# Optimization experiments

Measured on AMD Instinct MI355X. Metric: run time of the kernel, lower is better.

## Reference

```python
import jax, jax.numpy as jnp
import numpy as np

N_ENTITY = 64368
N_REL = 40
DIM = 128
N_BASES = 8
N_EDGES = 500000
BATCH = 64
SEED_LEN = 32


def _glorot(k, shape, gain=1.414):
    fan_in, fan_out = shape[0], shape[1]
    bound = gain * np.sqrt(6.0 / (fan_in + fan_out))
    return jax.random.uniform(k, shape, jnp.float32, -bound, bound)


def setup_inputs() -> dict:
    key = jax.random.key(0)
    ks = jax.random.split(key, 11)
    return dict(
        seed_ids=jax.random.randint(ks[0], (BATCH, SEED_LEN), 0, N_ENTITY),
        edge_src=jax.random.randint(ks[1], (N_EDGES,), 0, N_ENTITY),
        edge_dst=jax.random.randint(ks[2], (N_EDGES,), 0, N_ENTITY),
        edge_type=jax.random.randint(ks[3], (N_EDGES,), 0, N_REL),
        basis=jax.random.normal(ks[4], (N_BASES, N_ENTITY, DIM), jnp.float32) * 0.02,
        att=jax.random.normal(ks[5], (N_REL, N_BASES), jnp.float32) * 0.1,
        root=jax.random.normal(ks[6], (N_ENTITY, DIM), jnp.float32) * 0.02,
        rgcn_bias=jnp.zeros((DIM,), jnp.float32),
        attn_a=_glorot(ks[7], (DIM, DIM)),
        attn_b=_glorot(ks[8], (DIM, 1)),
        out_bias=jnp.zeros((N_ENTITY,), jnp.float32),
    )


def _rgcn_nodes(basis, att, root, rgcn_bias, edge_src, edge_dst, edge_type):
    # RGCNConv with x=None: message for edge e is row src[e] of w[type[e]],
    # where w = att @ basis (basis decomposition); 'mean' aggregation to dst;
    # update: aggr + root + bias.
    n_entity, dim = root.shape
    coeff = att[edge_type]  # [E, nb]
    agg = jnp.zeros((n_entity, dim), jnp.float32)
    for b in range(basis.shape[0]):  # small fixed loop over bases
        m = basis[b][edge_src] * coeff[:, b][:, None]  # [E, dim]
        agg = agg + jax.ops.segment_sum(m, edge_dst, num_segments=n_entity)
    deg = jax.ops.segment_sum(jnp.ones_like(edge_dst, jnp.float32), edge_dst,
                              num_segments=n_entity)
    agg = agg / jnp.maximum(deg, 1.0)[:, None]
    return agg + root + rgcn_bias[None, :]


def reference(seed_ids, edge_src, edge_dst, edge_type, basis, att, root,
              rgcn_bias, attn_a, attn_b, out_bias):
    nodes = _rgcn_nodes(basis, att, root, rgcn_bias, edge_src, edge_dst, edge_type)
    # self-attention pooling over each seed set (all entries valid / non-empty)
    H = nodes[seed_ids]  # [B, S, D]
    e = jnp.einsum('bsd,d->bs', jnp.tanh(jnp.einsum('bsd,de->bse', H, attn_a)),
                   attn_b[:, 0])  # [B, S]
    attn = jax.nn.softmax(e, axis=-1)
    u = jnp.einsum('bs,bsd->bd', attn, H)  # [B, D]
    # scores = F.linear(u, nodes_features, output.bias)
    scores = u @ nodes.T + out_bias[None, :]  # [B, n_entity]
    return scores
```

## Files before the change

kernel.cpp:

```cpp
#include <hip/hip_runtime.h>
#include <hip/hip_fp16.h>

#define N_ENTITY 64368
#define N_REL 40
#define DIM 128
#define N_BASES 8
#define N_EDGES 500000
#define BATCH 64
#define SEED_LEN 32
#define NROWS (BATCH * SEED_LEN)
#define SCAN_NB ((N_ENTITY + 255) / 256)
#define NPAD (SCAN_NB * 256)

#define CAP_S 40
#define CAP_D 40

struct alignas(8) half4 { __half2 lo, hi; };

__global__ __launch_bounds__(256) void k_scatter(
    const int* __restrict__ esrc, const int* __restrict__ edst,
    const int* __restrict__ etype, const float* __restrict__ basis,
    const float* __restrict__ att, int* __restrict__ cnts,
    int* __restrict__ cntd, int* __restrict__ slots,
    __half* __restrict__ msg, float* __restrict__ agg)
{
    int e = blockIdx.x * 256 + threadIdx.x;
    if (e >= N_EDGES) return;
    int s = esrc[e], d = edst[e], t = etype[e];

    int kd = atomicAdd(&cntd[d], 1);
    unsigned pack;
    if (kd < CAP_D) pack = ((unsigned)(d * CAP_D + kd) << 6) | (unsigned)t;
    else            pack = 0x80000000u | ((unsigned)d << 6) | (unsigned)t;

    int ks = atomicAdd(&cnts[s], 1);
    if (ks < CAP_S) {
        slots[(size_t)s * CAP_S + ks] = (int)pack;
    } else {
        const size_t bstride = (size_t)N_ENTITY * DIM;
        for (int dd = 0; dd < DIM; ++dd) {
            float m = 0.f;
            #pragma unroll
            for (int b = 0; b < N_BASES; ++b)
                m += att[t * N_BASES + b] * basis[b * bstride + (size_t)s * DIM + dd];
            if (kd < CAP_D)
                msg[(size_t)(d * CAP_D + kd) * DIM + dd] = __float2half(m);
            else
                unsafeAtomicAdd(&agg[(size_t)d * DIM + dd], m);
        }
    }
}

__global__ __launch_bounds__(256) void k_phaseA(
    const int* __restrict__ cnts, const int* __restrict__ slots,
    const float* __restrict__ basis, const float* __restrict__ att,
    __half* __restrict__ msg, float* __restrict__ agg)
{
    __shared__ float att_s[N_REL * N_BASES];
    int tid = threadIdx.x;
    for (int i = tid; i < N_REL * N_BASES; i += 256) att_s[i] = att[i];
    __syncthreads();

    int sid = (blockIdx.x * 256 + tid) >> 5;
    int l32 = tid & 31;
    if (sid >= N_ENTITY) return;
    int cnt = cnts[sid];
    if (cnt == 0) return;
    if (cnt > CAP_S) cnt = CAP_S;
    const int* sl = slots + (size_t)sid * CAP_S;

    const size_t bstride = (size_t)N_ENTITY * DIM;
    const float* bp = basis + (size_t)sid * DIM + l32 * 4;
    float4 r0 = *(const float4*)(bp + 0 * bstride);
    float4 r1 = *(const float4*)(bp + 1 * bstride);
    float4 r2 = *(const float4*)(bp + 2 * bstride);
    float4 r3 = *(const float4*)(bp + 3 * bstride);
    float4 r4 = *(const float4*)(bp + 4 * bstride);
    float4 r5 = *(const float4*)(bp + 5 * bstride);
    float4 r6 = *(const float4*)(bp + 6 * bstride);
    float4 r7 = *(const float4*)(bp + 7 * bstride);

    int j = 0;
    for (; j + 1 < cnt; j += 2) {
        int pA = sl[j];
        int pB = sl[j + 1];
        const float* cAp = att_s + (pA & 63) * N_BASES;
        const float* cBp = att_s + (pB & 63) * N_BASES;
        float4 cA0 = *(const float4*)(cAp);
        float4 cA1 = *(const float4*)(cAp + 4);
        float4 cB0 = *(const float4*)(cBp);
        float4 cB1 = *(const float4*)(cBp + 4);

        float4 mA, mB;
        mA.x = cA0.x*r0.x + cA0.y*r1.x + cA0.z*r2.x + cA0.w*r3.x
             + cA1.x*r4.x + cA1.y*r5.x + cA1.z*r6.x + cA1.w*r7.x;
        mA.y = cA0.x*r0.y + cA0.y*r1.y + cA0.z*r2.y + cA0.w*r3.y
             + cA1.x*r4.y + cA1.y*r5.y + cA1.z*r6.y + cA1.w*r7.y;
        mA.z = cA0.x*r0.z + cA0.y*r1.z + cA0.z*r2.z + cA0.w*r3.z
             + cA1.x*r4.z + cA1.y*r5.z + cA1.z*r6.z + cA1.w*r7.z;
        mA.w = cA0.x*r0.w + cA0.y*r1.w + cA0.z*r2.w + cA0.w*r3.w
             + cA1.x*r4.w + cA1.y*r5.w + cA1.z*r6.w + cA1.w*r7.w;
        mB.x = cB0.x*r0.x + cB0.y*r1.x + cB0.z*r2.x + cB0.w*r3.x
             + cB1.x*r4.x + cB1.y*r5.x + cB1.z*r6.x + cB1.w*r7.x;
        mB.y = cB0.x*r0.y + cB0.y*r1.y + cB0.z*r2.y + cB0.w*r3.y
             + cB1.x*r4.y + cB1.y*r5.y + cB1.z*r6.y + cB1.w*r7.y;
        mB.z = cB0.x*r0.z + cB0.y*r1.z + cB0.z*r2.z + cB0.w*r3.z
             + cB1.x*r4.z + cB1.y*r5.z + cB1.z*r6.z + cB1.w*r7.z;
        mB.w = cB0.x*r0.w + cB0.y*r1.w + cB0.z*r2.w + cB0.w*r3.w
             + cB1.x*r4.w + cB1.y*r5.w + cB1.z*r6.w + cB1.w*r7.w;

        half4 hA, hB;
        hA.lo = __floats2half2_rn(mA.x, mA.y);
        hA.hi = __floats2half2_rn(mA.z, mA.w);
        hB.lo = __floats2half2_rn(mB.x, mB.y);
        hB.hi = __floats2half2_rn(mB.z, mB.w);
        if (pA >= 0) {
            *(half4*)(msg + ((size_t)((unsigned)pA >> 6) << 7) + (l32 << 2)) = hA;
        } else {
            int dd = (int)(((unsigned)pA >> 6) & 0x1FFFFu);
            float* ap = agg + (size_t)dd * DIM + l32 * 4;
            unsafeAtomicAdd(ap + 0, mA.x); unsafeAtomicAdd(ap + 1, mA.y);
            unsafeAtomicAdd(ap + 2, mA.z); unsafeAtomicAdd(ap + 3, mA.w);
        }
        if (pB >= 0) {
            *(half4*)(msg + ((size_t)((unsigned)pB >> 6) << 7) + (l32 << 2)) = hB;
        } else {
            int dd = (int)(((unsigned)pB >> 6) & 0x1FFFFu);
            float* ap = agg + (size_t)dd * DIM + l32 * 4;
            unsafeAtomicAdd(ap + 0, mB.x); unsafeAtomicAdd(ap + 1, mB.y);
            unsafeAtomicAdd(ap + 2, mB.z); unsafeAtomicAdd(ap + 3, mB.w);
        }
    }
    if (j < cnt) {
        int pA = sl[j];
        const float* cAp = att_s + (pA & 63) * N_BASES;
        float4 cA0 = *(const float4*)(cAp);
        float4 cA1 = *(const float4*)(cAp + 4);
        float4 mA;
        mA.x = cA0.x*r0.x + cA0.y*r1.x + cA0.z*r2.x + cA0.w*r3.x
             + cA1.x*r4.x + cA1.y*r5.x + cA1.z*r6.x + cA1.w*r7.x;
        mA.y = cA0.x*r0.y + cA0.y*r1.y + cA0.z*r2.y + cA0.w*r3.y
             + cA1.x*r4.y + cA1.y*r5.y + cA1.z*r6.y + cA1.w*r7.y;
        mA.z = cA0.x*r0.z + cA0.y*r1.z + cA0.z*r2.z + cA0.w*r3.z
             + cA1.x*r4.z + cA1.y*r5.z + cA1.z*r6.z + cA1.w*r7.z;
        mA.w = cA0.x*r0.w + cA0.y*r1.w + cA0.z*r2.w + cA0.w*r3.w
             + cA1.x*r4.w + cA1.y*r5.w + cA1.z*r6.w + cA1.w*r7.w;
        half4 hA;
        hA.lo = __floats2half2_rn(mA.x, mA.y);
        hA.hi = __floats2half2_rn(mA.z, mA.w);
        if (pA >= 0) {
            *(half4*)(msg + ((size_t)((unsigned)pA >> 6) << 7) + (l32 << 2)) = hA;
        } else {
            int dd = (int)(((unsigned)pA >> 6) & 0x1FFFFu);
            float* ap = agg + (size_t)dd * DIM + l32 * 4;
            unsafeAtomicAdd(ap + 0, mA.x); unsafeAtomicAdd(ap + 1, mA.y);
            unsafeAtomicAdd(ap + 2, mA.z); unsafeAtomicAdd(ap + 3, mA.w);
        }
    }
}

__global__ __launch_bounds__(256) void k_phaseB(
    const int* __restrict__ cntd, const __half* __restrict__ msg,
    const float* __restrict__ root, const float* __restrict__ bias,
    float* __restrict__ agg)
{
    int wid  = (int)((blockIdx.x * 256 + threadIdx.x) >> 6);
    int lane = threadIdx.x & 63;
    if (wid >= N_ENTITY) return;
    int c = cntd[wid];
    int n = (c < CAP_D) ? c : CAP_D;
    const __half2* mp = (const __half2*)msg + (size_t)wid * (CAP_D * 64) + lane;

    float ax = 0.f, ay = 0.f;
    int j = 0;
    for (; j + 3 < n; j += 4) {
        float2 f0 = __half22float2(mp[(j + 0) * 64]);
        float2 f1 = __half22float2(mp[(j + 1) * 64]);
        float2 f2 = __half22float2(mp[(j + 2) * 64]);
        float2 f3 = __half22float2(mp[(j + 3) * 64]);
        ax += (f0.x + f1.x) + (f2.x + f3.x);
        ay += (f0.y + f1.y) + (f2.y + f3.y);
    }
    for (; j < n; ++j) {
        float2 f = __half22float2(mp[j * 64]);
        ax += f.x; ay += f.y;
    }

    int o = wid * DIM + lane * 2;
    float2 prev = *(const float2*)(agg + o);
    ax += prev.x; ay += prev.y;

    float inv = 1.0f / fmaxf((float)c, 1.0f);
    float2 r  = *(const float2*)(root + o);
    float2 bb = *(const float2*)(bias + lane * 2);
    float2 outv;
    outv.x = ax * inv + r.x + bb.x;
    outv.y = ay * inv + r.y + bb.y;
    *(float2*)(agg + o) = outv;
}

__global__ __launch_bounds__(256) void k_attn(
    const int* __restrict__ seed_ids, const float* __restrict__ nodes,
    const float* __restrict__ A, const float* __restrict__ Bv,
    float* __restrict__ uT)
{
    __shared__ float Hs[SEED_LEN * DIM];
    __shared__ float ew[SEED_LEN];
    __shared__ float attw[SEED_LEN];

    int b = blockIdx.x, tid = threadIdx.x;

    for (int i = tid; i < SEED_LEN * DIM; i += 256) {
        int ss = i >> 7, d = i & 127;
        Hs[i] = nodes[(size_t)seed_ids[b * SEED_LEN + ss] * DIM + d];
    }
    __syncthreads();

    int jx = tid & 31;
    int iy = tid >> 5;
    float acc[4][4] = {{0,0,0,0},{0,0,0,0},{0,0,0,0},{0,0,0,0}};

    for (int d = 0; d < DIM; ++d) {
        const float4 a4 = *(const float4*)(A + d * DIM + jx * 4);
        float h0 = Hs[(iy * 4 + 0) * DIM + d];
        float h1 = Hs[(iy * 4 + 1) * DIM + d];
        float h2 = Hs[(iy * 4 + 2) * DIM + d];
        float h3 = Hs[(iy * 4 + 3) * DIM + d];
        acc[0][0] += h0 * a4.x; acc[0][1] += h0 * a4.y;
        acc[0][2] += h0 * a4.z; acc[0][3] += h0 * a4.w;
        acc[1][0] += h1 * a4.x; acc[1][1] += h1 * a4.y;
        acc[1][2] += h1 * a4.z; acc[1][3] += h1 * a4.w;
        acc[2][0] += h2 * a4.x; acc[2][1] += h2 * a4.y;
        acc[2][2] += h2 * a4.z; acc[2][3] += h2 * a4.w;
        acc[3][0] += h3 * a4.x; acc[3][1] += h3 * a4.y;
        acc[3][2] += h3 * a4.z; acc[3][3] += h3 * a4.w;
    }

    const float4 bv = *(const float4*)(Bv + jx * 4);
    #pragma unroll
    for (int i = 0; i < 4; ++i) {
        float pe = tanhf(acc[i][0]) * bv.x + tanhf(acc[i][1]) * bv.y
                 + tanhf(acc[i][2]) * bv.z + tanhf(acc[i][3]) * bv.w;
        pe += __shfl_xor(pe, 1, 64);
        pe += __shfl_xor(pe, 2, 64);
        pe += __shfl_xor(pe, 4, 64);
        pe += __shfl_xor(pe, 8, 64);
        pe += __shfl_xor(pe, 16, 64);
        if (jx == 0) ew[iy * 4 + i] = pe;
    }
    __syncthreads();

    if (tid == 0) {
        float mx = -1e30f;
        for (int k = 0; k < SEED_LEN; ++k) mx = fmaxf(mx, ew[k]);
        float ssum = 0.0f;
        for (int k = 0; k < SEED_LEN; ++k) {
            float v = expf(ew[k] - mx);
            attw[k] = v; ssum += v;
        }
        float inv = 1.0f / ssum;
        for (int k = 0; k < SEED_LEN; ++k) attw[k] *= inv;
    }
    __syncthreads();

    if (tid < DIM) {
        float a = 0.0f;
        for (int k = 0; k < SEED_LEN; ++k) a += attw[k] * Hs[k * DIM + tid];
        uT[tid * BATCH + b] = a;
    }
}

__global__ __launch_bounds__(256) void k_scores(
    const float* __restrict__ nodes, const float* __restrict__ uT,
    const float* __restrict__ out_bias, float* __restrict__ out)
{
    __shared__ float Nl[DIM * 65];

    int tid = threadIdx.x;
    int n0  = blockIdx.x * 64;

    for (int i = tid; i < 64 * DIM; i += 256) {
        int n = i >> 7, d = i & 127;
        int gn = n0 + n;
        Nl[d * 65 + n] = (gn < N_ENTITY) ? nodes[(size_t)gn * DIM + d] : 0.0f;
    }
    __syncthreads();

    int w    = __builtin_amdgcn_readfirstlane(tid >> 6);
    int lane = tid & 63;
    int b0   = w * 16;

    float acc[16];
    #pragma unroll
    for (int k = 0; k < 16; ++k) acc[k] = 0.0f;

    #pragma unroll 4
    for (int d = 0; d < DIM; ++d) {
        float nv = Nl[d * 65 + lane];
        const float* up = uT + d * BATCH + b0;
        #pragma unroll
        for (int k = 0; k < 16; ++k) acc[k] += up[k] * nv;
    }

    int gn = n0 + lane;
    if (gn < N_ENTITY) {
        float ob = out_bias[gn];
        #pragma unroll
        for (int k = 0; k < 16; ++k)
            out[(size_t)(b0 + k) * N_ENTITY + gn] = acc[k] + ob;
    }
}

__global__ __launch_bounds__(256) void k_histF(
    const int* __restrict__ edst, int* __restrict__ hist)
{
    int e = blockIdx.x * 256 + threadIdx.x;
    if (e < N_EDGES) atomicAdd(&hist[edst[e]], 1);
}

__global__ __launch_bounds__(256) void k_scan1F(
    const int* __restrict__ hist, int* __restrict__ ptr,
    int* __restrict__ partial)
{
    __shared__ int s[256];
    int tid = threadIdx.x;
    int gid = blockIdx.x * 256 + tid;
    int v = hist[gid];
    s[tid] = v;
    __syncthreads();
    for (int off = 1; off < 256; off <<= 1) {
        int t = (tid >= off) ? s[tid - off] : 0;
        __syncthreads();
        s[tid] += t;
        __syncthreads();
    }
    ptr[gid] = s[tid] - v;
    if (tid == 255) partial[blockIdx.x] = s[255];
}

__global__ __launch_bounds__(256) void k_scan23F(
    int* __restrict__ ptr, const int* __restrict__ partial,
    int* __restrict__ work)
{
    __shared__ int s[256];
    int tid = threadIdx.x;
    int c   = blockIdx.x;
    int sum = 0;
    for (int k = tid; k < c; k += 256) sum += partial[k];
    s[tid] = sum;
    __syncthreads();
    for (int off = 128; off > 0; off >>= 1) {
        if (tid < off) s[tid] += s[tid + off];
        __syncthreads();
    }
    int p = ptr[c * 256 + tid] + s[0];
    ptr[c * 256 + tid]  = p;
    work[c * 256 + tid] = p;
}

__global__ __launch_bounds__(256) void k_scatterF(
    const int* __restrict__ esrc, const int* __restrict__ edst,
    const int* __restrict__ etype, int* __restrict__ work,
    int* __restrict__ meta)
{
    int e = blockIdx.x * 256 + threadIdx.x;
    if (e < N_EDGES) {
        int pos = atomicAdd(&work[edst[e]], 1);
        meta[pos] = esrc[e] * 64 + etype[e];
    }
}

#define ACC8(C0, C1, V0, V1, V2, V3, V4, V5, V6, V7)                         \
    acc.x += C0.x*V0.x + C0.y*V1.x + C0.z*V2.x + C0.w*V3.x                   \
           + C1.x*V4.x + C1.y*V5.x + C1.z*V6.x + C1.w*V7.x;                  \
    acc.y += C0.x*V0.y + C0.y*V1.y + C0.z*V2.y + C0.w*V3.y                   \
           + C1.x*V4.y + C1.y*V5.y + C1.z*V6.y + C1.w*V7.y;                  \
    acc.z += C0.x*V0.z + C0.y*V1.z + C0.z*V2.z + C0.w*V3.z                   \
           + C1.x*V4.z + C1.y*V5.z + C1.z*V6.z + C1.w*V7.z;                  \
    acc.w += C0.x*V0.w + C0.y*V1.w + C0.z*V2.w + C0.w*V3.w                   \
           + C1.x*V4.w + C1.y*V5.w + C1.z*V6.w + C1.w*V7.w;

__global__ __launch_bounds__(256) void k_gatherF(
    const int* __restrict__ ptr, const int* __restrict__ hist,
    const int* __restrict__ meta, const float* __restrict__ basis,
    const float* __restrict__ att, const float* __restrict__ root,
    const float* __restrict__ bias, float* __restrict__ agg)
{
    __shared__ float att_s[N_REL * N_BASES];
    int tid = threadIdx.x;
    for (int i = tid; i < N_REL * N_BASES; i += 256) att_s[i] = att[i];
    __syncthreads();

    int wid  = (int)((blockIdx.x * 256 + tid) >> 6);
    int lane = tid & 63;
    if (wid >= N_ENTITY) return;

    int half = lane >> 5;
    int l32  = lane & 31;
    int p   = ptr[wid];
    int cnt = hist[wid];
    const size_t bstride = (size_t)N_ENTITY * DIM;

    float4 acc = {0.f, 0.f, 0.f, 0.f};
    int j = 0;
    for (; j < cnt; j += 2) {
        int m0 = meta[p + j];
        bool has1 = (j + 1 < cnt);
        int m1 = has1 ? meta[p + j + 1] : m0;
        int m = half ? m1 : m0;
        float sc = (half && !has1) ? 0.0f : 1.0f;
        const float* bA = basis + (size_t)(m >> 6) * DIM + l32 * 4;
        float4 a0 = *(const float4*)(bA + 0 * bstride);
        float4 a1 = *(const float4*)(bA + 1 * bstride);
        float4 a2 = *(const float4*)(bA + 2 * bstride);
        float4 a3 = *(const float4*)(bA + 3 * bstride);
        float4 a4 = *(const float4*)(bA + 4 * bstride);
        float4 a5 = *(const float4*)(bA + 5 * bstride);
        float4 a6 = *(const float4*)(bA + 6 * bstride);
        float4 a7 = *(const float4*)(bA + 7 * bstride);
        float4 c0 = *(const float4*)(att_s + (m & 63) * N_BASES);
        float4 c1 = *(const float4*)(att_s + (m & 63) * N_BASES + 4);
        c0.x *= sc; c0.y *= sc; c0.z *= sc; c0.w *= sc;
        c1.x *= sc; c1.y *= sc; c1.z *= sc; c1.w *= sc;
        ACC8(c0, c1, a0, a1, a2, a3, a4, a5, a6, a7)
    }

    acc.x += __shfl_xor(acc.x, 32, 64);
    acc.y += __shfl_xor(acc.y, 32, 64);
    acc.z += __shfl_xor(acc.z, 32, 64);
    acc.w += __shfl_xor(acc.w, 32, 64);

    if (half == 0) {
        float inv = 1.0f / fmaxf((float)cnt, 1.0f);
        int o = wid * DIM + l32 * 4;
        float4 r  = *(const float4*)(root + o);
        float4 bb = *(const float4*)(bias + l32 * 4);
        float4 outv;
        outv.x = acc.x * inv + r.x + bb.x;
        outv.y = acc.y * inv + r.y + bb.y;
        outv.z = acc.z * inv + r.z + bb.z;
        outv.w = acc.w * inv + r.w + bb.w;
        *(float4*)(agg + o) = outv;
    }
}

extern "C" void kernel_launch(void* const* d_in, const int* in_sizes, int n_in,
                              void* d_out, int out_size, void* d_ws, size_t ws_size,
                              hipStream_t stream)
{
    const int*   seed_ids  = (const int*)d_in[0];
    const int*   esrc      = (const int*)d_in[1];
    const int*   edst      = (const int*)d_in[2];
    const int*   etype     = (const int*)d_in[3];
    const float* basis     = (const float*)d_in[4];
    const float* att       = (const float*)d_in[5];
    const float* root      = (const float*)d_in[6];
    const float* rgcn_bias = (const float*)d_in[7];
    const float* attn_a    = (const float*)d_in[8];
    const float* attn_b    = (const float*)d_in[9];
    const float* out_bias  = (const float*)d_in[10];
    float* out = (float*)d_out;

    const size_t AGG_F   = (size_t)N_ENTITY * DIM;
    const size_t SLOTS_W = (size_t)N_ENTITY * CAP_S;
    const size_t MSG_W   = (size_t)N_ENTITY * CAP_D * DIM / 2;

    const size_t main_words = AGG_F + 2 * NPAD + SLOTS_W + MSG_W
                            + 2 * BATCH * DIM + 64;
    bool big = ws_size >= main_words * 4;

    if (big) {
        float*  agg   = (float*)d_ws;
        int*    cntd  = (int*)(agg + AGG_F);
        int*    cnts  = cntd + NPAD;
        int*    slots = cnts + NPAD;
        __half* msg   = (__half*)(slots + SLOTS_W);
        float*  uT    = (float*)((int*)msg + MSG_W);

        hipMemsetAsync(d_ws, 0, (AGG_F + 2 * NPAD) * sizeof(int), stream);

        k_scatter<<<(N_EDGES + 255) / 256, 256, 0, stream>>>(
            esrc, edst, etype, basis, att, cnts, cntd, slots, msg, agg);
        k_phaseA<<<N_ENTITY / 8, 256, 0, stream>>>(
            cnts, slots, basis, att, msg, agg);
        k_phaseB<<<(N_ENTITY + 3) / 4, 256, 0, stream>>>(
            cntd, msg, root, rgcn_bias, agg);
        k_attn<<<BATCH, 256, 0, stream>>>(seed_ids, agg, attn_a, attn_b, uT);
        k_scores<<<(N_ENTITY + 63) / 64, 256, 0, stream>>>(agg, uT, out_bias, out);
    } else {
        float* agg   = (float*)d_ws;
        int*   hist  = (int*)(agg + AGG_F);
        int*   ptr   = hist + NPAD;
        int*   work  = ptr + NPAD;
        int*   part  = work + NPAD;
        int*   meta  = part + 256;
        float* uT    = (float*)(meta + N_EDGES);

        hipMemsetAsync(hist, 0, NPAD * sizeof(int), stream);
        k_histF<<<(N_EDGES + 255) / 256, 256, 0, stream>>>(edst, hist);
        k_scan1F<<<SCAN_NB, 256, 0, stream>>>(hist, ptr, part);
        k_scan23F<<<SCAN_NB, 256, 0, stream>>>(ptr, part, work);
        k_scatterF<<<(N_EDGES + 255) / 256, 256, 0, stream>>>(
            esrc, edst, etype, work, meta);
        k_gatherF<<<(N_ENTITY * 64 + 255) / 256, 256, 0, stream>>>(
            ptr, hist, meta, basis, att, root, rgcn_bias, agg);
        k_attn<<<BATCH, 256, 0, stream>>>(seed_ids, agg, attn_a, attn_b, uT);
        k_scores<<<(N_ENTITY + 63) / 64, 256, 0, stream>>>(agg, uT, out_bias, out);
    }
}
```

Measured before the change: 569.0 us.

## Route degree-overflow edges to overflow message rows instead of atomics into agg

Edges whose destination exceeds the per-node slot capacity now get a row in a small overflow message region plus a destination list, instead of atomically adding into agg. This removes the need to zero the whole agg buffer (the memset now covers only the counters) and drops atomics from phase A. Phase A is unrolled by four, and phase B reads 16-byte half8 vectors with four row groups per wave, reduced by shuffles. Every phase-B wave scans the overflow list linearly, which costs little when it is empty but grows with the overflow count. Overflow entries beyond the cap are clamped onto one slot, which would lose data.

New measurement: 578.0 us. No clear change (+1.6%).

```diff
diff --git a/kernel.cpp b/kernel.cpp
--- a/kernel.cpp
+++ b/kernel.cpp
@@ -14,28 +14,37 @@
 
 #define CAP_S 40
 #define CAP_D 40
-
-struct alignas(8) half4 { __half2 lo, hi; };
+#define OVF_CAP 4096
+
+struct alignas(8)  half4 { __half2 lo, hi; };
+struct alignas(16) h8    { __half2 a, b, c, d; };
 
 __global__ __launch_bounds__(256) void k_scatter(
     const int* __restrict__ esrc, const int* __restrict__ edst,
     const int* __restrict__ etype, const float* __restrict__ basis,
     const float* __restrict__ att, int* __restrict__ cnts,
-    int* __restrict__ cntd, int* __restrict__ slots,
-    __half* __restrict__ msg, float* __restrict__ agg)
+    int* __restrict__ cntd, int* __restrict__ novf, int* __restrict__ ovfd,
+    int* __restrict__ slots, __half* __restrict__ msg)
 {
     int e = blockIdx.x * 256 + threadIdx.x;
     if (e >= N_EDGES) return;
     int s = esrc[e], d = edst[e], t = etype[e];
 
     int kd = atomicAdd(&cntd[d], 1);
-    unsigned pack;
-    if (kd < CAP_D) pack = ((unsigned)(d * CAP_D + kd) << 6) | (unsigned)t;
-    else            pack = 0x80000000u | ((unsigned)d << 6) | (unsigned)t;
+    int row;
+    if (kd < CAP_D) {
+        row = d * CAP_D + kd;
+    } else {
+        int o = atomicAdd(novf, 1);
+        if (o >= OVF_CAP) o = OVF_CAP - 1;
+        ovfd[o] = d;
+        row = N_ENTITY * CAP_D + o;
+    }
+    int pack = (row << 6) | t;
 
     int ks = atomicAdd(&cnts[s], 1);
     if (ks < CAP_S) {
-        slots[(size_t)s * CAP_S + ks] = (int)pack;
+        slots[(size_t)s * CAP_S + ks] = pack;
     } else {
         const size_t bstride = (size_t)N_ENTITY * DIM;
         for (int dd = 0; dd < DIM; ++dd) {
@@ -43,18 +52,38 @@
             #pragma unroll
             for (int b = 0; b < N_BASES; ++b)
                 m += att[t * N_BASES + b] * basis[b * bstride + (size_t)s * DIM + dd];
-            if (kd < CAP_D)
-                msg[(size_t)(d * CAP_D + kd) * DIM + dd] = __float2half(m);
-            else
-                unsafeAtomicAdd(&agg[(size_t)d * DIM + dd], m);
+            msg[(size_t)row * DIM + dd] = __float2half(m);
         }
     }
 }
+
+#define MSG_ROW(pp, mm)                                                      \
+    {                                                                        \
+        const float* cp = att_s + ((pp) & 63) * N_BASES;                     \
+        float4 c0 = *(const float4*)(cp);                                    \
+        float4 c1 = *(const float4*)(cp + 4);                                \
+        mm.x = c0.x*r0.x + c0.y*r1.x + c0.z*r2.x + c0.w*r3.x                 \
+             + c1.x*r4.x + c1.y*r5.x + c1.z*r6.x + c1.w*r7.x;                \
+        mm.y = c0.x*r0.y + c0.y*r1.y + c0.z*r2.y + c0.w*r3.y                 \
+             + c1.x*r4.y + c1.y*r5.y + c1.z*r6.y + c1.w*r7.y;                \
+        mm.z = c0.x*r0.z + c0.y*r1.z + c0.z*r2.z + c0.w*r3.z                 \
+             + c1.x*r4.z + c1.y*r5.z + c1.z*r6.z + c1.w*r7.z;                \
+        mm.w = c0.x*r0.w + c0.y*r1.w + c0.z*r2.w + c0.w*r3.w                 \
+             + c1.x*r4.w + c1.y*r5.w + c1.z*r6.w + c1.w*r7.w;                \
+    }
+
+#define MSG_STORE(pp, mm)                                                    \
+    {                                                                        \
+        half4 h;                                                             \
+        h.lo = __floats2half2_rn(mm.x, mm.y);                                \
+        h.hi = __floats2half2_rn(mm.z, mm.w);                                \
+        *(half4*)(msg + ((size_t)((pp) >> 6) << 7) + (l32 << 2)) = h;        \
+    }
 
 __global__ __launch_bounds__(256) void k_phaseA(
     const int* __restrict__ cnts, const int* __restrict__ slots,
     const float* __restrict__ basis, const float* __restrict__ att,
-    __half* __restrict__ msg, float* __restrict__ agg)
+    __half* __restrict__ msg)
 {
     __shared__ float att_s[N_REL * N_BASES];
     int tid = threadIdx.x;
@@ -81,121 +110,93 @@
     float4 r7 = *(const float4*)(bp + 7 * bstride);
 
     int j = 0;
-    for (; j + 1 < cnt; j += 2) {
-        int pA = sl[j];
-        int pB = sl[j + 1];
-        const float* cAp = att_s + (pA & 63) * N_BASES;
-        const float* cBp = att_s + (pB & 63) * N_BASES;
-        float4 cA0 = *(const float4*)(cAp);
-        float4 cA1 = *(const float4*)(cAp + 4);
-        float4 cB0 = *(const float4*)(cBp);
-        float4 cB1 = *(const float4*)(cBp + 4);
-
-        float4 mA, mB;
-        mA.x = cA0.x*r0.x + cA0.y*r1.x + cA0.z*r2.x + cA0.w*r3.x
-             + cA1.x*r4.x + cA1.y*r5.x + cA1.z*r6.x + cA1.w*r7.x;
-        mA.y = cA0.x*r0.y + cA0.y*r1.y + cA0.z*r2.y + cA0.w*r3.y
-             + cA1.x*r4.y + cA1.y*r5.y + cA1.z*r6.y + cA1.w*r7.y;
-        mA.z = cA0.x*r0.z + cA0.y*r1.z + cA0.z*r2.z + cA0.w*r3.z
-             + cA1.x*r4.z + cA1.y*r5.z + cA1.z*r6.z + cA1.w*r7.z;
-        mA.w = cA0.x*r0.w + cA0.y*r1.w + cA0.z*r2.w + cA0.w*r3.w
-             + cA1.x*r4.w + cA1.y*r5.w + cA1.z*r6.w + cA1.w*r7.w;
-        mB.x = cB0.x*r0.x + cB0.y*r1.x + cB0.z*r2.x + cB0.w*r3.x
-             + cB1.x*r4.x + cB1.y*r5.x + cB1.z*r6.x + cB1.w*r7.x;
-        mB.y = cB0.x*r0.y + cB0.y*r1.y + cB0.z*r2.y + cB0.w*r3.y
-             + cB1.x*r4.y + cB1.y*r5.y + cB1.z*r6.y + cB1.w*r7.y;
-        mB.z = cB0.x*r0.z + cB0.y*r1.z + cB0.z*r2.z + cB0.w*r3.z
-             + cB1.x*r4.z + cB1.y*r5.z + cB1.z*r6.z + cB1.w*r7.z;
-        mB.w = cB0.x*r0.w + cB0.y*r1.w + cB0.z*r2.w + cB0.w*r3.w
-             + cB1.x*r4.w + cB1.y*r5.w + cB1.z*r6.w + cB1.w*r7.w;
-
-        half4 hA, hB;
-        hA.lo = __floats2half2_rn(mA.x, mA.y);
-        hA.hi = __floats2half2_rn(mA.z, mA.w);
-        hB.lo = __floats2half2_rn(mB.x, mB.y);
-        hB.hi = __floats2half2_rn(mB.z, mB.w);
-        if (pA >= 0) {
-            *(half4*)(msg + ((size_t)((unsigned)pA >> 6) << 7) + (l32 << 2)) = hA;
-        } else {
-            int dd = (int)(((unsigned)pA >> 6) & 0x1FFFFu);
-            float* ap = agg + (size_t)dd * DIM + l32 * 4;
-            unsafeAtomicAdd(ap + 0, mA.x); unsafeAtomicAdd(ap + 1, mA.y);
-            unsafeAtomicAdd(ap + 2, mA.z); unsafeAtomicAdd(ap + 3, mA.w);
-        }
-        if (pB >= 0) {
-            *(half4*)(msg + ((size_t)((unsigned)pB >> 6) << 7) + (l32 << 2)) = hB;
-        } else {
-            int dd = (int)(((unsigned)pB >> 6) & 0x1FFFFu);
-            float* ap = agg + (size_t)dd * DIM + l32 * 4;
-            unsafeAtomicAdd(ap + 0, mB.x); unsafeAtomicAdd(ap + 1, mB.y);
-            unsafeAtomicAdd(ap + 2, mB.z); unsafeAtomicAdd(ap + 3, mB.w);
-        }
-    }
-    if (j < cnt) {
-        int pA = sl[j];
-        const float* cAp = att_s + (pA & 63) * N_BASES;
-        float4 cA0 = *(const float4*)(cAp);
-        float4 cA1 = *(const float4*)(cAp + 4);
-        float4 mA;
-        mA.x = cA0.x*r0.x + cA0.y*r1.x + cA0.z*r2.x + cA0.w*r3.x
-             + cA1.x*r4.x + cA1.y*r5.x + cA1.z*r6.x + cA1.w*r7.x;
-        mA.y = cA0.x*r0.y + cA0.y*r1.y + cA0.z*r2.y + cA0.w*r3.y
-             + cA1.x*r4.y + cA1.y*r5.y + cA1.z*r6.y + cA1.w*r7.y;
-        mA.z = cA0.x*r0.z + cA0.y*r1.z + cA0.z*r2.z + cA0.w*r3.z
-             + cA1.x*r4.z + cA1.y*r5.z + cA1.z*r6.z + cA1.w*r7.z;
-        mA.w = cA0.x*r0.w + cA0.y*r1.w + cA0.z*r2.w + cA0.w*r3.w
-             + cA1.x*r4.w + cA1.y*r5.w + cA1.z*r6.w + cA1.w*r7.w;
-        half4 hA;
-        hA.lo = __floats2half2_rn(mA.x, mA.y);
-        hA.hi = __floats2half2_rn(mA.z, mA.w);
-        if (pA >= 0) {
-            *(half4*)(msg + ((size_t)((unsigned)pA >> 6) << 7) + (l32 << 2)) = hA;
-        } else {
-            int dd = (int)(((unsigned)pA >> 6) & 0x1FFFFu);
-            float* ap = agg + (size_t)dd * DIM + l32 * 4;
-            unsafeAtomicAdd(ap + 0, mA.x); unsafeAtomicAdd(ap + 1, mA.y);
-            unsafeAtomicAdd(ap + 2, mA.z); unsafeAtomicAdd(ap + 3, mA.w);
-        }
+    for (; j + 3 < cnt; j += 4) {
+        int p0 = sl[j], p1 = sl[j + 1], p2 = sl[j + 2], p3 = sl[j + 3];
+        float4 m0, m1, m2, m3;
+        MSG_ROW(p0, m0) MSG_ROW(p1, m1) MSG_ROW(p2, m2) MSG_ROW(p3, m3)
+        MSG_STORE(p0, m0) MSG_STORE(p1, m1) MSG_STORE(p2, m2) MSG_STORE(p3, m3)
+    }
+    for (; j < cnt; ++j) {
+        int p0 = sl[j];
+        float4 m0;
+        MSG_ROW(p0, m0)
+        MSG_STORE(p0, m0)
     }
 }
 
 __global__ __launch_bounds__(256) void k_phaseB(
-    const int* __restrict__ cntd, const __half* __restrict__ msg,
+    const int* __restrict__ cntd, const int* __restrict__ novf,
+    const int* __restrict__ ovfd, const __half* __restrict__ msg,
     const float* __restrict__ root, const float* __restrict__ bias,
     float* __restrict__ agg)
 {
     int wid  = (int)((blockIdx.x * 256 + threadIdx.x) >> 6);
     int lane = threadIdx.x & 63;
     if (wid >= N_ENTITY) return;
+    int g = lane >> 4;
+    int q = lane & 15;
+
     int c = cntd[wid];
     int n = (c < CAP_D) ? c : CAP_D;
-    const __half2* mp = (const __half2*)msg + (size_t)wid * (CAP_D * 64) + lane;
-
-    float ax = 0.f, ay = 0.f;
-    int j = 0;
-    for (; j + 3 < n; j += 4) {
-        float2 f0 = __half22float2(mp[(j + 0) * 64]);
-        float2 f1 = __half22float2(mp[(j + 1) * 64]);
-        float2 f2 = __half22float2(mp[(j + 2) * 64]);
-        float2 f3 = __half22float2(mp[(j + 3) * 64]);
-        ax += (f0.x + f1.x) + (f2.x + f3.x);
-        ay += (f0.y + f1.y) + (f2.y + f3.y);
-    }
-    for (; j < n; ++j) {
-        float2 f = __half22float2(mp[j * 64]);
-        ax += f.x; ay += f.y;
-    }
-
-    int o = wid * DIM + lane * 2;
-    float2 prev = *(const float2*)(agg + o);
-    ax += prev.x; ay += prev.y;
+    const __half* base = msg + (size_t)wid * (CAP_D * DIM) + (q << 3);
+
+    float a0 = 0.f, a1 = 0.f, a2 = 0.f, a3 = 0.f;
+    float a4 = 0.f, a5 = 0.f, a6 = 0.f, a7 = 0.f;
+    for (int j = 0; j < n; j += 4) {
+        int r = j + g;
+        h8 v = *(const h8*)(base + ((size_t)r << 7));
+        bool ok = (r < n);
+        float2 f0 = __half22float2(v.a);
+        float2 f1 = __half22float2(v.b);
+        float2 f2 = __half22float2(v.c);
+        float2 f3 = __half22float2(v.d);
+        if (ok) {
+            a0 += f0.x; a1 += f0.y; a2 += f1.x; a3 += f1.y;
+            a4 += f2.x; a5 += f2.y; a6 += f3.x; a7 += f3.y;
+        }
+    }
+
+    int nov = *novf;
+    if (nov > 0) {
+        if (nov > OVF_CAP) nov = OVF_CAP;
+        for (int k = 0; k < nov; ++k) {
+            if (ovfd[k] == wid && g == 0) {
+                const __half* p = msg + ((size_t)(N_ENTITY * CAP_D) + k) * DIM
+                                + (q << 3);
+                h8 v = *(const h8*)p;
+                float2 f0 = __half22float2(v.a);
+                float2 f1 = __half22float2(v.b);
+                float2 f2 = __half22float2(v.c);
+                float2 f3 = __half22float2(v.d);
+                a0 += f0.x; a1 += f0.y; a2 += f1.x; a3 += f1.y;
+                a4 += f2.x; a5 += f2.y; a6 += f3.x; a7 += f3.y;
+            }
+        }
+    }
+
+    a0 += __shfl_xor(a0, 16, 64); a0 += __shfl_xor(a0, 32, 64);
+    a1 += __shfl_xor(a1, 16, 64); a1 += __shfl_xor(a1, 32, 64);
+    a2 += __shfl_xor(a2, 16, 64); a2 += __shfl_xor(a2, 32, 64);
+    a3 += __shfl_xor(a3, 16, 64); a3 += __shfl_xor(a3, 32, 64);
+    a4 += __shfl_xor(a4, 16, 64); a4 += __shfl_xor(a4, 32, 64);
+    a5 += __shfl_xor(a5, 16, 64); a5 += __shfl_xor(a5, 32, 64);
+    a6 += __shfl_xor(a6, 16, 64); a6 += __shfl_xor(a6, 32, 64);
+    a7 += __shfl_xor(a7, 16, 64); a7 += __shfl_xor(a7, 32, 64);
+
+    float vx, vy;
+    if      (g == 0) { vx = a0; vy = a1; }
+    else if (g == 1) { vx = a2; vy = a3; }
+    else if (g == 2) { vx = a4; vy = a5; }
+    else             { vx = a6; vy = a7; }
 
     float inv = 1.0f / fmaxf((float)c, 1.0f);
+    int dof = (q << 3) + (g << 1);
+    int o = wid * DIM + dof;
     float2 r  = *(const float2*)(root + o);
-    float2 bb = *(const float2*)(bias + lane * 2);
+    float2 bb = *(const float2*)(bias + dof);
     float2 outv;
-    outv.x = ax * inv + r.x + bb.x;
-    outv.y = ay * inv + r.y + bb.y;
+    outv.x = vx * inv + r.x + bb.x;
+    outv.y = vy * inv + r.y + bb.y;
     *(float2*)(agg + o) = outv;
 }
 
@@ -463,28 +464,30 @@
 
     const size_t AGG_F   = (size_t)N_ENTITY * DIM;
     const size_t SLOTS_W = (size_t)N_ENTITY * CAP_S;
-    const size_t MSG_W   = (size_t)N_ENTITY * CAP_D * DIM / 2;
-
-    const size_t main_words = AGG_F + 2 * NPAD + SLOTS_W + MSG_W
-                            + 2 * BATCH * DIM + 64;
+    const size_t MSG_W   = ((size_t)N_ENTITY * CAP_D + OVF_CAP) * DIM / 2;
+
+    const size_t main_words = AGG_F + 2 * NPAD + 16 + OVF_CAP + SLOTS_W
+                            + MSG_W + 2 * BATCH * DIM + 64;
     bool big = ws_size >= main_words * 4;
 
     if (big) {
         float*  agg   = (float*)d_ws;
         int*    cntd  = (int*)(agg + AGG_F);
         int*    cnts  = cntd + NPAD;
-        int*    slots = cnts + NPAD;
+        int*    novf  = cnts + NPAD;
+        int*    ovfd  = novf + 16;
+        int*    slots = ovfd + OVF_CAP;
         __half* msg   = (__half*)(slots + SLOTS_W);
         float*  uT    = (float*)((int*)msg + MSG_W);
 
-        hipMemsetAsync(d_ws, 0, (AGG_F + 2 * NPAD) * sizeof(int), stream);
+        hipMemsetAsync(cntd, 0, (2 * NPAD + 16) * sizeof(int), stream);
 
         k_scatter<<<(N_EDGES + 255) / 256, 256, 0, stream>>>(
-            esrc, edst, etype, basis, att, cnts, cntd, slots, msg, agg);
+            esrc, edst, etype, basis, att, cnts, cntd, novf, ovfd, slots, msg);
         k_phaseA<<<N_ENTITY / 8, 256, 0, stream>>>(
-            cnts, slots, basis, att, msg, agg);
+            cnts, slots, basis, att, msg);
         k_phaseB<<<(N_ENTITY + 3) / 4, 256, 0, stream>>>(
-            cntd, msg, root, rgcn_bias, agg);
+            cntd, novf, ovfd, msg, root, rgcn_bias, agg);
         k_attn<<<BATCH, 256, 0, stream>>>(seed_ids, agg, attn_a, attn_b, uT);
         k_scores<<<(N_ENTITY + 63) / 64, 256, 0, stream>>>(agg, uT, out_bias, out);
     } else {
```
